# Kernel tuning notes

Measured on AMD Instinct MI355X. Metric: run time of the kernel, lower is better.

Reference implementation:

```python
import jax, jax.numpy as jnp
import numpy as np

CUTOFF = 10.0
EPS_W = 1e-5
EPS_LN = 1e-5

def _silu(v):
    return v * jax.nn.sigmoid(v)

def setup_inputs() -> dict:
    key = jax.random.key(0)
    ks = jax.random.split(key, 12)
    N, E, H, R = 50000, 300000, 256, 64
    s = lambda fan_in: 1.0 / np.sqrt(fan_in)
    inp = {
        'x': jax.random.normal(ks[0], (N, H), jnp.float32),
        'edge_index': jax.random.randint(ks[1], (2, E), 0, N, jnp.int64 if jax.config.jax_enable_x64 else jnp.int32),
        'distances': jax.random.uniform(ks[2], (E,), jnp.float32) * CUTOFF,
        'centers': jnp.linspace(0.0, CUTOFF, R).astype(jnp.float32),
        'widths': jnp.full((R,), CUTOFF / R, jnp.float32),
        'rbf_w1': jax.random.normal(ks[3], (R, R), jnp.float32) * s(R),
        'rbf_b1': jnp.zeros((R,), jnp.float32),
        'rbf_w2': jax.random.normal(ks[4], (R, R), jnp.float32) * s(R),
        'rbf_b2': jnp.zeros((R,), jnp.float32),
        'filt_w1': jax.random.normal(ks[5], (R, H), jnp.float32) * s(R),
        'filt_b1': jnp.zeros((H,), jnp.float32),
        'filt_w2': jax.random.normal(ks[6], (H, H), jnp.float32) * s(H),
        'filt_b2': jnp.zeros((H,), jnp.float32),
        'filt_w3': jax.random.normal(ks[7], (H, H), jnp.float32) * s(H),
        'filt_b3': jnp.zeros((H,), jnp.float32),
        'node_w': jax.random.normal(ks[8], (H, H), jnp.float32) * s(H),
        'node_b': jnp.zeros((H,), jnp.float32),
        'ln_g': jnp.ones((H,), jnp.float32),
        'ln_b': jnp.zeros((H,), jnp.float32),
        'gate_w': jax.random.normal(ks[9], (H, H), jnp.float32) * s(H),
        'gate_b': jnp.zeros((H,), jnp.float32),
    }
    return inp

def reference(x, edge_index, distances, centers, widths,
              rbf_w1, rbf_b1, rbf_w2, rbf_b2,
              filt_w1, filt_b1, filt_w2, filt_b2, filt_w3, filt_b3,
              node_w, node_b, ln_g, ln_b, gate_w, gate_b):
    # LearnableRBF: envelope * gaussian basis, then 2-layer SiLU proj
    d = distances
    env = 0.5 * (jnp.cos(d * jnp.pi / CUTOFF) + 1.0) * (d < CUTOFF).astype(x.dtype)  # [E]
    rbf = jnp.exp(-0.5 * ((d[:, None] - centers) / (jnp.abs(widths) + EPS_W)) ** 2)   # [E,R]
    r = rbf * env[:, None]
    r = _silu(r @ rbf_w1 + rbf_b1) @ rbf_w2 + rbf_b2                                  # [E,R]
    # filter network: Lin-SiLU-Lin-SiLU-Lin
    W = _silu(r @ filt_w1 + filt_b1)
    W = _silu(W @ filt_w2 + filt_b2) @ filt_w3 + filt_b3                              # [E,H]
    # gather -> modulate -> scatter-add (CFConv messaging)
    row, col = edge_index[0], edge_index[1]
    msg = (x[col] @ node_w + node_b) * W                                              # [E,H]
    agg = jax.ops.segment_sum(msg, row, num_segments=x.shape[0])                      # [N,H]
    h = x + agg
    mu = jnp.mean(h, axis=-1, keepdims=True)
    var = jnp.var(h, axis=-1, keepdims=True)
    out = (h - mu) / jnp.sqrt(var + EPS_LN) * ln_g + ln_b
    return out * jax.nn.sigmoid(out @ gate_w + gate_b)
```

## Files before the change

kernel.cpp:

```cpp
#include <hip/hip_runtime.h>
#include <hip/hip_bf16.h>
#include <math.h>

typedef __attribute__((ext_vector_type(8))) short bf16x8;
typedef __attribute__((ext_vector_type(4))) float f32x4;
typedef unsigned short ushort_t;

constexpr float F_CUTOFF = 10.0f;
constexpr float F_EPS_W  = 1e-5f;
constexpr float F_EPS_LN = 1e-5f;
constexpr float F_PI     = 3.14159265358979323846f;

__device__ __forceinline__ float silu_f(float v)   { return v / (1.0f + __expf(-v)); }
__device__ __forceinline__ float sigmoid_f(float v){ return 1.0f / (1.0f + __expf(-v)); }

__device__ __forceinline__ ushort_t f2bf(float f) {
    union { __hip_bfloat16 h; ushort_t u; } v; v.h = __float2bfloat16(f); return v.u;
}
__device__ __forceinline__ float bf2f(ushort_t u) {
    union { __hip_bfloat16 h; ushort_t u; } v; v.u = u; return __bfloat162float(v.h);
}

__device__ __forceinline__ float f4c(const float4& v, int q) {
    return q == 0 ? v.x : q == 1 ? v.y : q == 2 ? v.z : v.w;
}

__global__ void count_kernel(const int* __restrict__ eidx, int* __restrict__ cnt, int E)
{
    int e = blockIdx.x * 256 + threadIdx.x;
    if (e < E) atomicAdd(&cnt[eidx[e]], 1);
}

__global__ __launch_bounds__(1024)
void scan_kernel(const int* __restrict__ cnt, int* __restrict__ start,
                 int* __restrict__ cursor, int N)
{
    __shared__ int part[1024];
    const int tid = threadIdx.x;
    const int C = (N + 1023) >> 10;
    const int base = tid * C;
    int s = 0;
    for (int i = 0; i < C; ++i) {
        int idx = base + i;
        if (idx < N) s += cnt[idx];
    }
    part[tid] = s;
    __syncthreads();
    for (int off = 1; off < 1024; off <<= 1) {
        int v = (tid >= off) ? part[tid - off] : 0;
        __syncthreads();
        part[tid] += v;
        __syncthreads();
    }
    int run = part[tid] - s;
    for (int i = 0; i < C; ++i) {
        int idx = base + i;
        if (idx < N) {
            start[idx]  = run;
            cursor[idx] = run;
            run += cnt[idx];
        }
    }
    if (tid == 1023) start[N] = part[1023];
}

__global__ void scatter_kernel(const int* __restrict__ eidx, int* __restrict__ cursor,
                               int* __restrict__ slot, int E)
{
    int e = blockIdx.x * 256 + threadIdx.x;
    if (e < E) slot[e] = atomicAdd(&cursor[eidx[e]], 1);
}

__global__ void cvt_transpose_kernel(const float* __restrict__ in, ushort_t* __restrict__ out,
                                     int K, int N, int logK)
{
    int idx = blockIdx.x * 256 + threadIdx.x;
    if (idx >= K * N) return;
    int n = idx >> logK;
    int k = idx & (K - 1);
    out[idx] = f2bf(in[k * N + n]);
}

__global__ void combine_w_kernel(const float* __restrict__ w2, const float* __restrict__ fw1,
                                 ushort_t* __restrict__ out)
{
    int idx = blockIdx.x * 256 + threadIdx.x;
    int c = idx >> 6, j = idx & 63;
    float s = 0.f;
    #pragma unroll 8
    for (int n = 0; n < 64; ++n) s += w2[j * 64 + n] * fw1[n * 256 + c];
    out[idx] = f2bf(s);
}

__global__ void combine_b_kernel(const float* __restrict__ b2, const float* __restrict__ fw1,
                                 const float* __restrict__ fb1, float* __restrict__ out)
{
    int c = threadIdx.x;
    float s = fb1[c];
    #pragma unroll 8
    for (int n = 0; n < 64; ++n) s += b2[n] * fw1[n * 256 + c];
    out[c] = s;
}

__global__ __launch_bounds__(256)
void gemm256_bf16_kernel(const float* __restrict__ A, const float* __restrict__ Wm,
                         const float* __restrict__ bias, ushort_t* __restrict__ out, int M)
{
    __shared__ float4 As4[64][64];
    const int t = threadIdx.x;
    const int row0 = blockIdx.x * 64;

    #pragma unroll
    for (int i = 0; i < 16; ++i) {
        int flat = t + i * 256;
        int r = flat >> 6, k4 = flat & 63;
        int row = row0 + r;
        float4 v = make_float4(0.f, 0.f, 0.f, 0.f);
        if (row < M) v = reinterpret_cast<const float4*>(A)[row * 64 + k4];
        As4[r][k4] = v;
    }
    __syncthreads();

    const int jt  = t & 31;
    const int et  = t >> 5;
    const int j04 = jt * 2;
    const int r0  = et * 8;

    float acc[8][8];
    #pragma unroll
    for (int r = 0; r < 8; ++r)
        #pragma unroll
        for (int c = 0; c < 8; ++c) acc[r][c] = 0.f;

    for (int k4 = 0; k4 < 64; ++k4) {
        float4 a4[8];
        #pragma unroll
        for (int r = 0; r < 8; ++r) a4[r] = As4[r0 + r][k4];
        #pragma unroll
        for (int q = 0; q < 4; ++q) {
            const int k = k4 * 4 + q;
            float4 b0 = reinterpret_cast<const float4*>(Wm)[k * 64 + j04];
            float4 b1 = reinterpret_cast<const float4*>(Wm)[k * 64 + j04 + 1];
            float bb[8] = {b0.x, b0.y, b0.z, b0.w, b1.x, b1.y, b1.z, b1.w};
            #pragma unroll
            for (int r = 0; r < 8; ++r) {
                float av = f4c(a4[r], q);
                #pragma unroll
                for (int c = 0; c < 8; ++c) acc[r][c] = fmaf(av, bb[c], acc[r][c]);
            }
        }
    }

    float4 bv0 = reinterpret_cast<const float4*>(bias)[j04];
    float4 bv1 = reinterpret_cast<const float4*>(bias)[j04 + 1];
    float bb[8] = {bv0.x, bv0.y, bv0.z, bv0.w, bv1.x, bv1.y, bv1.z, bv1.w};

    #pragma unroll
    for (int r = 0; r < 8; ++r) {
        int row = row0 + r0 + r;
        if (row >= M) continue;
        ushort_t o8[8];
        #pragma unroll
        for (int c = 0; c < 8; ++c) o8[c] = f2bf(acc[r][c] + bb[c]);
        *reinterpret_cast<uint4*>(out + (size_t)row * 256 + jt * 8) = *reinterpret_cast<uint4*>(o8);
    }
}

__global__ __launch_bounds__(256)
void gate_gemm_kernel(const float* __restrict__ A, const float* __restrict__ Wm,
                      const float* __restrict__ bias, float* __restrict__ out, int M)
{
    __shared__ float4 As4[64][64];
    const int t = threadIdx.x;
    const int row0 = blockIdx.x * 64;

    #pragma unroll
    for (int i = 0; i < 16; ++i) {
        int flat = t + i * 256;
        int r = flat >> 6, k4 = flat & 63;
        int row = row0 + r;
        float4 v = make_float4(0.f, 0.f, 0.f, 0.f);
        if (row < M) v = reinterpret_cast<const float4*>(A)[row * 64 + k4];
        As4[r][k4] = v;
    }
    __syncthreads();

    const int jt  = t & 31;
    const int et  = t >> 5;
    const int j04 = jt * 2;
    const int r0  = et * 8;

    float acc[8][8];
    #pragma unroll
    for (int r = 0; r < 8; ++r)
        #pragma unroll
        for (int c = 0; c < 8; ++c) acc[r][c] = 0.f;

    for (int k4 = 0; k4 < 64; ++k4) {
        float4 a4[8];
        #pragma unroll
        for (int r = 0; r < 8; ++r) a4[r] = As4[r0 + r][k4];
        #pragma unroll
        for (int q = 0; q < 4; ++q) {
            const int k = k4 * 4 + q;
            float4 b0 = reinterpret_cast<const float4*>(Wm)[k * 64 + j04];
            float4 b1 = reinterpret_cast<const float4*>(Wm)[k * 64 + j04 + 1];
            float bb[8] = {b0.x, b0.y, b0.z, b0.w, b1.x, b1.y, b1.z, b1.w};
            #pragma unroll
            for (int r = 0; r < 8; ++r) {
                float av = f4c(a4[r], q);
                #pragma unroll
                for (int c = 0; c < 8; ++c) acc[r][c] = fmaf(av, bb[c], acc[r][c]);
            }
        }
    }

    float4 bv0 = reinterpret_cast<const float4*>(bias)[j04];
    float4 bv1 = reinterpret_cast<const float4*>(bias)[j04 + 1];
    float bb[8] = {bv0.x, bv0.y, bv0.z, bv0.w, bv1.x, bv1.y, bv1.z, bv1.w};

    #pragma unroll
    for (int r = 0; r < 8; ++r) {
        int row = row0 + r0 + r;
        if (row >= M) continue;
        float4 a0 = As4[r0 + r][j04];
        float4 a1 = As4[r0 + r][j04 + 1];
        float aa[8] = {a0.x, a0.y, a0.z, a0.w, a1.x, a1.y, a1.z, a1.w};
        float o[8];
        #pragma unroll
        for (int c = 0; c < 8; ++c) o[c] = aa[c] * sigmoid_f(acc[r][c] + bb[c]);
        reinterpret_cast<float4*>(out)[row * 64 + j04]     = make_float4(o[0], o[1], o[2], o[3]);
        reinterpret_cast<float4*>(out)[row * 64 + j04 + 1] = make_float4(o[4], o[5], o[6], o[7]);
    }
}

template<int KS, int NT, bool SILU>
__device__ __forceinline__ void mlp_stage(const unsigned char* in, unsigned char* out,
                                          const ushort_t* __restrict__ Wt,
                                          const float* __restrict__ bias,
                                          int wn, int g, int q)
{
    constexpr int K = KS * 32;
    f32x4 acc[2][NT];
    #pragma unroll
    for (int mt = 0; mt < 2; ++mt)
        #pragma unroll
        for (int nt = 0; nt < NT; ++nt) acc[mt][nt] = (f32x4){0.f, 0.f, 0.f, 0.f};

    #pragma unroll
    for (int kk = 0; kk < KS; ++kk) {
        bf16x8 b[NT];
        #pragma unroll
        for (int nt = 0; nt < NT; ++nt) {
            int n = (wn * NT + nt) * 16 + q;
            b[nt] = *reinterpret_cast<const bf16x8*>(Wt + n * K + kk * 32 + g * 8);
        }
        bf16x8 a[2];
        #pragma unroll
        for (int mt = 0; mt < 2; ++mt) {
            int m = mt * 16 + q;
            int unit = (4 * kk + g) ^ (m & 7);
            a[mt] = *reinterpret_cast<const bf16x8*>(in + m * 512 + unit * 16);
        }
        #pragma unroll
        for (int mt = 0; mt < 2; ++mt)
            #pragma unroll
            for (int nt = 0; nt < NT; ++nt)
                acc[mt][nt] = __builtin_amdgcn_mfma_f32_16x16x32_bf16(a[mt], b[nt], acc[mt][nt], 0, 0, 0);
    }

    const bool evenq = (q & 1) == 0;
    #pragma unroll
    for (int nt = 0; nt < NT; ++nt) {
        int n0  = (wn * NT + nt) * 16 + q;
        int n_e = n0 & ~1;
        float2 bv = *reinterpret_cast<const float2*>(bias + n_e);
        #pragma unroll
        for (int mt = 0; mt < 2; ++mt) {
            float v[4], p[4];
            #pragma unroll
            for (int r = 0; r < 4; ++r) { v[r] = acc[mt][nt][r]; p[r] = __shfl_xor(v[r], 1, 64); }
            #pragma unroll
            for (int rr = 0; rr < 2; ++rr) {
                int r = evenq ? rr : (2 + rr);
                float lo = (evenq ? v[r] : p[r]) + bv.x;
                float hi = (evenq ? p[r] : v[r]) + bv.y;
                if (SILU) { lo = silu_f(lo); hi = silu_f(hi); }
                int m = mt * 16 + 4 * g + r;
                unsigned u = (unsigned)f2bf(lo) | ((unsigned)f2bf(hi) << 16);
                int byte = m * 512 + (((n_e >> 3) ^ (m & 7)) << 4) + ((n_e & 7) * 2);
                *reinterpret_cast<unsigned*>(out + byte) = u;
            }
        }
    }
}

template<int TWO>
__global__ __launch_bounds__(256, 4)
void edge_mfma_kernel(const float* __restrict__ dist, const int* __restrict__ eidx,
                      const float* __restrict__ centers, const float* __restrict__ widths,
                      const ushort_t* __restrict__ wt_rbf1, const float* __restrict__ rbf_b1,
                      const ushort_t* __restrict__ wt_comb, const float* __restrict__ b_comb,
                      const ushort_t* __restrict__ wt_f2, const float* __restrict__ filt_b2,
                      const ushort_t* __restrict__ wt_f3, const float* __restrict__ filt_b3,
                      const ushort_t* __restrict__ y, const int* __restrict__ slot,
                      float* __restrict__ dst, int E)
{
    __shared__ __align__(16) unsigned char bufA[16384];
    __shared__ __align__(16) unsigned char bufB[16384];
    __shared__ int rs_s[32];

    const int t  = threadIdx.x;
    const int e0 = blockIdx.x * 32;
    const int wn   = t >> 6;
    const int lane = t & 63;
    const int g = lane >> 4, q = lane & 15;

    if (t < 32) {
        int ge = e0 + t;
        if (TWO) rs_s[t] = (ge < E) ? slot[ge] : 0;
        else     rs_s[t] = (ge < E) ? eidx[ge] : 0;
    }

    const int e_own  = t >> 3;
    const int chunk  = t & 7;
    const int ge_own = e0 + e_own;
    const int col_own = (ge_own < E) ? eidx[E + ge_own] : 0;
    uint4 yv[4];
    #pragma unroll
    for (int i = 0; i < 4; ++i)
        yv[i] = *reinterpret_cast<const uint4*>(y + (size_t)col_own * 256 + (i * 8 + chunk) * 8);

    {
        float d = (ge_own < E) ? dist[ge_own] : F_CUTOFF;
        float env = (d < F_CUTOFF) ? 0.5f * (__cosf(d * (F_PI / F_CUTOFF)) + 1.0f) : 0.0f;
        unsigned char* rowp = bufA + e_own * 512;
        int k0 = chunk * 8;
        #pragma unroll
        for (int i = 0; i < 4; ++i) {
            int n = k0 + 2 * i;
            float c0 = centers[n],     w0 = fabsf(widths[n]) + F_EPS_W;
            float c1 = centers[n + 1], w1 = fabsf(widths[n + 1]) + F_EPS_W;
            float z0 = (d - c0) / w0, z1 = (d - c1) / w1;
            float r0 = env * __expf(-0.5f * z0 * z0);
            float r1 = env * __expf(-0.5f * z1 * z1);
            unsigned u = (unsigned)f2bf(r0) | ((unsigned)f2bf(r1) << 16);
            int byte = (((n >> 3) ^ (e_own & 7)) << 4) + ((n & 7) * 2);
            *reinterpret_cast<unsigned*>(rowp + byte) = u;
        }
    }
    __syncthreads();

    mlp_stage<2, 1, true>(bufA, bufB, wt_rbf1, rbf_b1, wn, g, q);
    __syncthreads();
    mlp_stage<2, 4, true>(bufB, bufA, wt_comb, b_comb, wn, g, q);
    __syncthreads();
    mlp_stage<8, 4, true>(bufA, bufB, wt_f2, filt_b2, wn, g, q);
    __syncthreads();

    #pragma unroll
    for (int i = 0; i < 4; ++i)
        *reinterpret_cast<uint4*>(bufA + e_own * 512 + (i * 8 + chunk) * 16) = yv[i];
    __syncthreads();

    {
        f32x4 acc[2][4];
        #pragma unroll
        for (int mt = 0; mt < 2; ++mt)
            #pragma unroll
            for (int nt = 0; nt < 4; ++nt) acc[mt][nt] = (f32x4){0.f, 0.f, 0.f, 0.f};

        #pragma unroll
        for (int kk = 0; kk < 8; ++kk) {
            bf16x8 b[4];
            #pragma unroll
            for (int nt = 0; nt < 4; ++nt) {
                int n = (wn * 4 + nt) * 16 + q;
                b[nt] = *reinterpret_cast<const bf16x8*>(wt_f3 + n * 256 + kk * 32 + g * 8);
            }
            bf16x8 a[2];
            #pragma unroll
            for (int mt = 0; mt < 2; ++mt) {
                int m = mt * 16 + q;
                int unit = (4 * kk + g) ^ (m & 7);
                a[mt] = *reinterpret_cast<const bf16x8*>(bufB + m * 512 + unit * 16);
            }
            #pragma unroll
            for (int mt = 0; mt < 2; ++mt)
                #pragma unroll
                for (int nt = 0; nt < 4; ++nt)
                    acc[mt][nt] = __builtin_amdgcn_mfma_f32_16x16x32_bf16(a[mt], b[nt], acc[mt][nt], 0, 0, 0);
        }

        float bn[4];
        int   nn[4];
        #pragma unroll
        for (int nt = 0; nt < 4; ++nt) { nn[nt] = (wn * 4 + nt) * 16 + q; bn[nt] = filt_b3[nn[nt]]; }

        #pragma unroll
        for (int mt = 0; mt < 2; ++mt) {
            #pragma unroll
            for (int r = 0; r < 4; ++r) {
                int m  = mt * 16 + 4 * g + r;
                int ge = e0 + m;
                if (ge < E) {
                    const unsigned char* yrow = bufA + m * 512;
                    if (TWO) {
                        float* mrow = dst + (size_t)rs_s[m] * 256;
                        #pragma unroll
                        for (int nt = 0; nt < 4; ++nt) {
                            float wv = acc[mt][nt][r] + bn[nt];
                            float yvv = bf2f(*reinterpret_cast<const ushort_t*>(yrow + nn[nt] * 2));
                            mrow[nn[nt]] = wv * yvv;
                        }
                    } else {
                        float* arow = dst + (size_t)rs_s[m] * 256;
                        #pragma unroll
                        for (int nt = 0; nt < 4; ++nt) {
                            float wv = acc[mt][nt][r] + bn[nt];
                            float yvv = bf2f(*reinterpret_cast<const ushort_t*>(yrow + nn[nt] * 2));
                            unsafeAtomicAdd(&arow[nn[nt]], wv * yvv);
                        }
                    }
                }
            }
        }
    }
}

__global__ __launch_bounds__(256)
void agg_ln_kernel(const float* __restrict__ x, const float* __restrict__ msg,
                   const int* __restrict__ start,
                   const float* __restrict__ g, const float* __restrict__ b,
                   float* __restrict__ out0, int N)
{
    int lane = threadIdx.x & 63;
    int row  = blockIdx.x * 4 + (threadIdx.x >> 6);
    if (row >= N) return;
    int s0 = start[row], s1 = start[row + 1];
    float4 h = reinterpret_cast<const float4*>(x)[row * 64 + lane];
    for (int s = s0; s < s1; ++s) {
        float4 m = reinterpret_cast<const float4*>(msg)[(size_t)s * 64 + lane];
        h.x += m.x; h.y += m.y; h.z += m.z; h.w += m.w;
    }
    float su  = h.x + h.y + h.z + h.w;
    float s2 = h.x * h.x + h.y * h.y + h.z * h.z + h.w * h.w;
    #pragma unroll
    for (int off = 32; off > 0; off >>= 1) {
        su += __shfl_xor(su, off, 64);
        s2 += __shfl_xor(s2, off, 64);
    }
    float mu  = su * (1.0f / 256.0f);
    float var = s2 * (1.0f / 256.0f) - mu * mu;
    float inv = rsqrtf(var + F_EPS_LN);
    float4 gv = reinterpret_cast<const float4*>(g)[lane];
    float4 bv = reinterpret_cast<const float4*>(b)[lane];
    float4 o;
    o.x = (h.x - mu) * inv * gv.x + bv.x;
    o.y = (h.y - mu) * inv * gv.y + bv.y;
    o.z = (h.z - mu) * inv * gv.z + bv.z;
    o.w = (h.w - mu) * inv * gv.w + bv.w;
    reinterpret_cast<float4*>(out0)[row * 64 + lane] = o;
}

__global__ __launch_bounds__(256)
void ln_kernel(const float* __restrict__ x, const float* __restrict__ agg,
               const float* __restrict__ g, const float* __restrict__ b,
               float* __restrict__ out0, int N)
{
    int lane = threadIdx.x & 63;
    int row  = blockIdx.x * 4 + (threadIdx.x >> 6);
    if (row >= N) return;
    float4 hx = reinterpret_cast<const float4*>(x)[row * 64 + lane];
    float4 ha = reinterpret_cast<const float4*>(agg)[row * 64 + lane];
    float4 h  = make_float4(hx.x + ha.x, hx.y + ha.y, hx.z + ha.z, hx.w + ha.w);
    float s  = h.x + h.y + h.z + h.w;
    float s2 = h.x * h.x + h.y * h.y + h.z * h.z + h.w * h.w;
    #pragma unroll
    for (int off = 32; off > 0; off >>= 1) {
        s  += __shfl_xor(s,  off, 64);
        s2 += __shfl_xor(s2, off, 64);
    }
    float mu  = s * (1.0f / 256.0f);
    float var = s2 * (1.0f / 256.0f) - mu * mu;
    float inv = rsqrtf(var + F_EPS_LN);
    float4 gv = reinterpret_cast<const float4*>(g)[lane];
    float4 bv = reinterpret_cast<const float4*>(b)[lane];
    float4 o;
    o.x = (h.x - mu) * inv * gv.x + bv.x;
    o.y = (h.y - mu) * inv * gv.y + bv.y;
    o.z = (h.z - mu) * inv * gv.z + bv.z;
    o.w = (h.w - mu) * inv * gv.w + bv.w;
    reinterpret_cast<float4*>(out0)[row * 64 + lane] = o;
}

extern "C" void kernel_launch(void* const* d_in, const int* in_sizes, int n_in,
                              void* d_out, int out_size, void* d_ws, size_t ws_size,
                              hipStream_t stream)
{
    const float* x       = (const float*)d_in[0];
    const int*   eidx    = (const int*)  d_in[1];
    const float* dist    = (const float*)d_in[2];
    const float* centers = (const float*)d_in[3];
    const float* widths  = (const float*)d_in[4];
    const float* rbf_w1  = (const float*)d_in[5];
    const float* rbf_b1  = (const float*)d_in[6];
    const float* rbf_w2  = (const float*)d_in[7];
    const float* rbf_b2  = (const float*)d_in[8];
    const float* filt_w1 = (const float*)d_in[9];
    const float* filt_b1 = (const float*)d_in[10];
    const float* filt_w2 = (const float*)d_in[11];
    const float* filt_b2 = (const float*)d_in[12];
    const float* filt_w3 = (const float*)d_in[13];
    const float* filt_b3 = (const float*)d_in[14];
    const float* node_w  = (const float*)d_in[15];
    const float* node_b  = (const float*)d_in[16];
    const float* ln_g    = (const float*)d_in[17];
    const float* ln_b    = (const float*)d_in[18];
    const float* gate_w  = (const float*)d_in[19];
    const float* gate_b  = (const float*)d_in[20];

    const int N = in_sizes[0] / 256;
    const int E = in_sizes[2];

    char* wsb = (char*)d_ws;
    size_t off = 0;
    auto alloc = [&](size_t bytes, size_t align) -> char* {
        off = (off + align - 1) & ~(align - 1);
        char* p = wsb + off;
        off += bytes;
        return p;
    };
    ushort_t* y_bf  = (ushort_t*)alloc((size_t)N * 256 * 2, 16);
    ushort_t* wt1   = (ushort_t*)alloc(64 * 64 * 2, 16);
    ushort_t* wcomb = (ushort_t*)alloc(256 * 64 * 2, 16);
    ushort_t* wf2   = (ushort_t*)alloc(256 * 256 * 2, 16);
    ushort_t* wf3   = (ushort_t*)alloc(256 * 256 * 2, 16);
    float*    bcomb = (float*)   alloc(256 * 4, 16);
    int*      cnt   = (int*)     alloc((size_t)N * 4, 16);
    int*      start = (int*)     alloc(((size_t)N + 1) * 4, 16);
    int*      cursor= (int*)     alloc((size_t)N * 4, 16);
    int*      slot  = (int*)     alloc((size_t)E * 4, 16);
    float*    msg   = (float*)   alloc((size_t)E * 256 * 4, 1024);
    const bool two_phase = (off <= ws_size);

    dim3 b256(256);

    cvt_transpose_kernel<<<dim3((64 * 64 + 255) / 256),   b256, 0, stream>>>(rbf_w1,  wt1, 64, 64, 6);
    combine_w_kernel<<<dim3(64), b256, 0, stream>>>(rbf_w2, filt_w1, wcomb);
    combine_b_kernel<<<dim3(1), b256, 0, stream>>>(rbf_b2, filt_w1, filt_b1, bcomb);
    cvt_transpose_kernel<<<dim3((256 * 256 + 255) / 256), b256, 0, stream>>>(filt_w2, wf2, 256, 256, 8);
    cvt_transpose_kernel<<<dim3((256 * 256 + 255) / 256), b256, 0, stream>>>(filt_w3, wf3, 256, 256, 8);

    gemm256_bf16_kernel<<<dim3((N + 63) / 64), b256, 0, stream>>>(x, node_w, node_b, y_bf, N);

    if (two_phase) {
        hipMemsetAsync(cnt, 0, (size_t)N * 4, stream);
        count_kernel<<<dim3((E + 255) / 256), b256, 0, stream>>>(eidx, cnt, E);
        scan_kernel<<<dim3(1), 1024, 0, stream>>>(cnt, start, cursor, N);
        scatter_kernel<<<dim3((E + 255) / 256), b256, 0, stream>>>(eidx, cursor, slot, E);

        edge_mfma_kernel<1><<<dim3((E + 31) / 32), b256, 0, stream>>>(
            dist, eidx, centers, widths,
            wt1, rbf_b1, wcomb, bcomb,
            wf2, filt_b2, wf3, filt_b3,
            y_bf, slot, msg, E);

        agg_ln_kernel<<<dim3((N + 3) / 4), b256, 0, stream>>>(x, msg, start, ln_g, ln_b, (float*)d_out, N);
    } else {
        hipMemsetAsync(d_out, 0, (size_t)out_size * sizeof(float), stream);
        edge_mfma_kernel<0><<<dim3((E + 31) / 32), b256, 0, stream>>>(
            dist, eidx, centers, widths,
            wt1, rbf_b1, wcomb, bcomb,
            wf2, filt_b2, wf3, filt_b3,
            y_bf, slot, (float*)d_out, E);
        ln_kernel<<<dim3((N + 3) / 4), b256, 0, stream>>>(x, (float*)d_out, ln_g, ln_b, (float*)d_out, N);
    }

    gate_gemm_kernel<<<dim3((N + 63) / 64), b256, 0, stream>>>((float*)d_out, gate_w, gate_b, (float*)d_out, N);
}
```

Baseline: 822.8 us.

## Split fused edge MLP into staged GEMM kernels with bf16 intermediates

Splits the monolithic per-edge kernel into an RBF/first-layer kernel that writes bf16 features, then two standalone 64-row tiled MFMA GEMM kernels with double-buffered LDS for the 256x256 filter layers. The last GEMM writes the bf16 filter into CSR-sorted slots, and the aggregation kernel gathers y by a sorted column array to do the multiply there. This replaces the fp32 message buffer with bf16 and gives larger GEMM tiles with better weight reuse. In exchange it adds extra global round trips of E x 256 bf16 intermediates and more kernel launches.

```diff
diff --git a/kernel.cpp b/kernel.cpp
--- a/kernel.cpp
+++ b/kernel.cpp
@@ -18,7 +18,7 @@
     union { __hip_bfloat16 h; ushort_t u; } v; v.h = __float2bfloat16(f); return v.u;
 }
 __device__ __forceinline__ float bf2f(ushort_t u) {
-    union { __hip_bfloat16 h; ushort_t u; } v; v.u = u; return __bfloat162float(v.h);
+    union { unsigned u; float f; } v; v.u = ((unsigned)u) << 16; return v.f;
 }
 
 __device__ __forceinline__ float f4c(const float4& v, int q) {
@@ -32,8 +32,8 @@
 }
 
 __global__ __launch_bounds__(1024)
-void scan_kernel(const int* __restrict__ cnt, int* __restrict__ start,
-                 int* __restrict__ cursor, int N)
+void scan_kernel(int* __restrict__ cnt ,
+                 int* __restrict__ start, int N)
 {
     __shared__ int part[1024];
     const int tid = threadIdx.x;
@@ -56,19 +56,24 @@
     for (int i = 0; i < C; ++i) {
         int idx = base + i;
         if (idx < N) {
-            start[idx]  = run;
-            cursor[idx] = run;
-            run += cnt[idx];
+            int c = cnt[idx];
+            start[idx] = run;
+            cnt[idx]   = run;
+            run += c;
         }
     }
     if (tid == 1023) start[N] = part[1023];
 }
 
 __global__ void scatter_kernel(const int* __restrict__ eidx, int* __restrict__ cursor,
-                               int* __restrict__ slot, int E)
+                               int* __restrict__ slot, int* __restrict__ colos, int E)
 {
     int e = blockIdx.x * 256 + threadIdx.x;
-    if (e < E) slot[e] = atomicAdd(&cursor[eidx[e]], 1);
+    if (e < E) {
+        int s = atomicAdd(&cursor[eidx[e]], 1);
+        slot[e] = s;
+        colos[s] = eidx[E + e];
+    }
 }
 
 __global__ void cvt_transpose_kernel(const float* __restrict__ in, ushort_t* __restrict__ out,
@@ -295,20 +300,15 @@
     }
 }
 
-template<int TWO>
 __global__ __launch_bounds__(256, 4)
-void edge_mfma_kernel(const float* __restrict__ dist, const int* __restrict__ eidx,
-                      const float* __restrict__ centers, const float* __restrict__ widths,
-                      const ushort_t* __restrict__ wt_rbf1, const float* __restrict__ rbf_b1,
-                      const ushort_t* __restrict__ wt_comb, const float* __restrict__ b_comb,
-                      const ushort_t* __restrict__ wt_f2, const float* __restrict__ filt_b2,
-                      const ushort_t* __restrict__ wt_f3, const float* __restrict__ filt_b3,
-                      const ushort_t* __restrict__ y, const int* __restrict__ slot,
-                      float* __restrict__ dst, int E)
+void rbf_f1_kernel(const float* __restrict__ dist,
+                   const float* __restrict__ centers, const float* __restrict__ widths,
+                   const ushort_t* __restrict__ wt_rbf1, const float* __restrict__ rbf_b1,
+                   const ushort_t* __restrict__ wt_comb, const float* __restrict__ b_comb,
+                   ushort_t* __restrict__ f1, int E)
 {
     __shared__ __align__(16) unsigned char bufA[16384];
     __shared__ __align__(16) unsigned char bufB[16384];
-    __shared__ int rs_s[32];
 
     const int t  = threadIdx.x;
     const int e0 = blockIdx.x * 32;
@@ -316,20 +316,9 @@
     const int lane = t & 63;
     const int g = lane >> 4, q = lane & 15;
 
-    if (t < 32) {
-        int ge = e0 + t;
-        if (TWO) rs_s[t] = (ge < E) ? slot[ge] : 0;
-        else     rs_s[t] = (ge < E) ? eidx[ge] : 0;
-    }
-
     const int e_own  = t >> 3;
     const int chunk  = t & 7;
     const int ge_own = e0 + e_own;
-    const int col_own = (ge_own < E) ? eidx[E + ge_own] : 0;
-    uint4 yv[4];
-    #pragma unroll
-    for (int i = 0; i < 4; ++i)
-        yv[i] = *reinterpret_cast<const uint4*>(y + (size_t)col_own * 256 + (i * 8 + chunk) * 8);
 
     {
         float d = (ge_own < E) ? dist[ge_own] : F_CUTOFF;
@@ -355,73 +344,115 @@
     __syncthreads();
     mlp_stage<2, 4, true>(bufB, bufA, wt_comb, b_comb, wn, g, q);
     __syncthreads();
-    mlp_stage<8, 4, true>(bufA, bufB, wt_f2, filt_b2, wn, g, q);
-    __syncthreads();
-
-    #pragma unroll
-    for (int i = 0; i < 4; ++i)
-        *reinterpret_cast<uint4*>(bufA + e_own * 512 + (i * 8 + chunk) * 16) = yv[i];
-    __syncthreads();
-
-    {
-        f32x4 acc[2][4];
-        #pragma unroll
-        for (int mt = 0; mt < 2; ++mt)
-            #pragma unroll
-            for (int nt = 0; nt < 4; ++nt) acc[mt][nt] = (f32x4){0.f, 0.f, 0.f, 0.f};
-
-        #pragma unroll
-        for (int kk = 0; kk < 8; ++kk) {
+
+    if (ge_own < E) {
+        #pragma unroll
+        for (int i = 0; i < 4; ++i) {
+            int c = chunk + i * 8;
+            int u = (c ^ (e_own & 7)) | (c & 24);
+            u = (c & 24) | ((c ^ (e_own & 7)) & 7);
+            uint4 v = *reinterpret_cast<const uint4*>(bufA + e_own * 512 + u * 16);
+            *reinterpret_cast<uint4*>(f1 + (size_t)ge_own * 256 + c * 8) = v;
+        }
+    }
+}
+
+template<int EPI>
+__global__ __launch_bounds__(256, 3)
+void gemm_stage_kernel(const ushort_t* __restrict__ A, const ushort_t* __restrict__ Wt,
+                       const float* __restrict__ bias, ushort_t* __restrict__ out,
+                       const int* __restrict__ slot, int M)
+{
+    __shared__ __align__(16) unsigned char sbuf[2][8192];
+    __shared__ int slot_s[64];
+
+    const int t  = threadIdx.x;
+    const int m0 = blockIdx.x * 64;
+    const int wn   = t >> 6;
+    const int lane = t & 63;
+    const int g = lane >> 4, q = lane & 15;
+
+    if (EPI == 1 && t < 64) {
+        int gm = m0 + t;
+        slot_s[t] = (gm < M) ? slot[gm] : 0;
+    }
+
+    const int s0r = t >> 3,        s0u = t & 7;
+    const int s1r = (t + 256) >> 3, s1u = t & 7;
+    const ushort_t* src0base = A + (size_t)((m0 + s0r < M) ? (m0 + s0r) : (M - 1)) * 256 + ((s0u ^ (s0r & 7)) * 8);
+    const ushort_t* src1base = A + (size_t)((m0 + s1r < M) ? (m0 + s1r) : (M - 1)) * 256 + ((s1u ^ (s1r & 7)) * 8);
+
+    uint4 p0 = *reinterpret_cast<const uint4*>(src0base);
+    uint4 p1 = *reinterpret_cast<const uint4*>(src1base);
+    *reinterpret_cast<uint4*>(&sbuf[0][t * 16])         = p0;
+    *reinterpret_cast<uint4*>(&sbuf[0][(t + 256) * 16]) = p1;
+    __syncthreads();
+
+    f32x4 acc[4][4];
+    #pragma unroll
+    for (int mt = 0; mt < 4; ++mt)
+        #pragma unroll
+        for (int nt = 0; nt < 4; ++nt) acc[mt][nt] = (f32x4){0.f, 0.f, 0.f, 0.f};
+
+    for (int kt = 0; kt < 4; ++kt) {
+        const int cur = kt & 1;
+        uint4 nx0, nx1;
+        if (kt < 3) {
+            nx0 = *reinterpret_cast<const uint4*>(src0base + (kt + 1) * 64);
+            nx1 = *reinterpret_cast<const uint4*>(src1base + (kt + 1) * 64);
+        }
+        #pragma unroll
+        for (int ks = 0; ks < 2; ++ks) {
             bf16x8 b[4];
             #pragma unroll
             for (int nt = 0; nt < 4; ++nt) {
-                int n = (wn * 4 + nt) * 16 + q;
-                b[nt] = *reinterpret_cast<const bf16x8*>(wt_f3 + n * 256 + kk * 32 + g * 8);
-            }
-            bf16x8 a[2];
-            #pragma unroll
-            for (int mt = 0; mt < 2; ++mt) {
-                int m = mt * 16 + q;
-                int unit = (4 * kk + g) ^ (m & 7);
-                a[mt] = *reinterpret_cast<const bf16x8*>(bufB + m * 512 + unit * 16);
-            }
-            #pragma unroll
-            for (int mt = 0; mt < 2; ++mt)
+                int n = wn * 64 + nt * 16 + q;
+                b[nt] = *reinterpret_cast<const bf16x8*>(Wt + (size_t)n * 256 + kt * 64 + ks * 32 + g * 8);
+            }
+            bf16x8 a[4];
+            #pragma unroll
+            for (int mt = 0; mt < 4; ++mt) {
+                int r = mt * 16 + q;
+                int u = (ks * 4 + g) ^ (r & 7);
+                a[mt] = *reinterpret_cast<const bf16x8*>(&sbuf[cur][r * 128 + u * 16]);
+            }
+            #pragma unroll
+            for (int mt = 0; mt < 4; ++mt)
                 #pragma unroll
                 for (int nt = 0; nt < 4; ++nt)
                     acc[mt][nt] = __builtin_amdgcn_mfma_f32_16x16x32_bf16(a[mt], b[nt], acc[mt][nt], 0, 0, 0);
         }
-
-        float bn[4];
-        int   nn[4];
-        #pragma unroll
-        for (int nt = 0; nt < 4; ++nt) { nn[nt] = (wn * 4 + nt) * 16 + q; bn[nt] = filt_b3[nn[nt]]; }
-
-        #pragma unroll
-        for (int mt = 0; mt < 2; ++mt) {
-            #pragma unroll
-            for (int r = 0; r < 4; ++r) {
-                int m  = mt * 16 + 4 * g + r;
-                int ge = e0 + m;
-                if (ge < E) {
-                    const unsigned char* yrow = bufA + m * 512;
-                    if (TWO) {
-                        float* mrow = dst + (size_t)rs_s[m] * 256;
-                        #pragma unroll
-                        for (int nt = 0; nt < 4; ++nt) {
-                            float wv = acc[mt][nt][r] + bn[nt];
-                            float yvv = bf2f(*reinterpret_cast<const ushort_t*>(yrow + nn[nt] * 2));
-                            mrow[nn[nt]] = wv * yvv;
-                        }
-                    } else {
-                        float* arow = dst + (size_t)rs_s[m] * 256;
-                        #pragma unroll
-                        for (int nt = 0; nt < 4; ++nt) {
-                            float wv = acc[mt][nt][r] + bn[nt];
-                            float yvv = bf2f(*reinterpret_cast<const ushort_t*>(yrow + nn[nt] * 2));
-                            unsafeAtomicAdd(&arow[nn[nt]], wv * yvv);
-                        }
-                    }
+        __syncthreads();
+        if (kt < 3) {
+            *reinterpret_cast<uint4*>(&sbuf[cur ^ 1][t * 16])         = nx0;
+            *reinterpret_cast<uint4*>(&sbuf[cur ^ 1][(t + 256) * 16]) = nx1;
+            __syncthreads();
+        }
+    }
+
+    const bool evenq = (q & 1) == 0;
+    #pragma unroll
+    for (int nt = 0; nt < 4; ++nt) {
+        int n0  = wn * 64 + nt * 16 + q;
+        int n_e = n0 & ~1;
+        float2 bv = *reinterpret_cast<const float2*>(bias + n_e);
+        #pragma unroll
+        for (int mt = 0; mt < 4; ++mt) {
+            float v[4], p[4];
+            #pragma unroll
+            for (int r = 0; r < 4; ++r) { v[r] = acc[mt][nt][r]; p[r] = __shfl_xor(v[r], 1, 64); }
+            #pragma unroll
+            for (int rr = 0; rr < 2; ++rr) {
+                int r = evenq ? rr : (2 + rr);
+                float lo = (evenq ? v[r] : p[r]) + bv.x;
+                float hi = (evenq ? p[r] : v[r]) + bv.y;
+                if (EPI == 0) { lo = silu_f(lo); hi = silu_f(hi); }
+                int mloc = mt * 16 + 4 * g + r;
+                int grow = m0 + mloc;
+                if (grow < M) {
+                    int drow = (EPI == 1) ? slot_s[mloc] : grow;
+                    unsigned u = (unsigned)f2bf(lo) | ((unsigned)f2bf(hi) << 16);
+                    *reinterpret_cast<unsigned*>(out + (size_t)drow * 256 + n_e) = u;
                 }
             }
         }
@@ -429,22 +460,29 @@
 }
 
 __global__ __launch_bounds__(256)
-void agg_ln_kernel(const float* __restrict__ x, const float* __restrict__ msg,
-                   const int* __restrict__ start,
-                   const float* __restrict__ g, const float* __restrict__ b,
-                   float* __restrict__ out0, int N)
+void agg_ln2_kernel(const float* __restrict__ x, const ushort_t* __restrict__ Wf,
+                    const int* __restrict__ start, const int* __restrict__ colos,
+                    const ushort_t* __restrict__ y,
+                    const float* __restrict__ g, const float* __restrict__ b,
+                    float* __restrict__ out0, int N)
 {
     int lane = threadIdx.x & 63;
     int row  = blockIdx.x * 4 + (threadIdx.x >> 6);
     if (row >= N) return;
     int s0 = start[row], s1 = start[row + 1];
-    float4 h = reinterpret_cast<const float4*>(x)[row * 64 + lane];
+    float4 hx = reinterpret_cast<const float4*>(x)[row * 64 + lane];
+    float hh[4] = {hx.x, hx.y, hx.z, hx.w};
     for (int s = s0; s < s1; ++s) {
-        float4 m = reinterpret_cast<const float4*>(msg)[(size_t)s * 64 + lane];
-        h.x += m.x; h.y += m.y; h.z += m.z; h.w += m.w;
-    }
-    float su  = h.x + h.y + h.z + h.w;
-    float s2 = h.x * h.x + h.y * h.y + h.z * h.z + h.w * h.w;
+        uint2 wv = *reinterpret_cast<const uint2*>(Wf + (size_t)s * 256 + lane * 4);
+        int c = colos[s];
+        uint2 yv = *reinterpret_cast<const uint2*>(y + (size_t)c * 256 + lane * 4);
+        hh[0] += bf2f((ushort_t)(wv.x & 0xffff)) * bf2f((ushort_t)(yv.x & 0xffff));
+        hh[1] += bf2f((ushort_t)(wv.x >> 16))    * bf2f((ushort_t)(yv.x >> 16));
+        hh[2] += bf2f((ushort_t)(wv.y & 0xffff)) * bf2f((ushort_t)(yv.y & 0xffff));
+        hh[3] += bf2f((ushort_t)(wv.y >> 16))    * bf2f((ushort_t)(yv.y >> 16));
+    }
+    float su = hh[0] + hh[1] + hh[2] + hh[3];
+    float s2 = hh[0]*hh[0] + hh[1]*hh[1] + hh[2]*hh[2] + hh[3]*hh[3];
     #pragma unroll
     for (int off = 32; off > 0; off >>= 1) {
         su += __shfl_xor(su, off, 64);
@@ -456,11 +494,131 @@
     float4 gv = reinterpret_cast<const float4*>(g)[lane];
     float4 bv = reinterpret_cast<const float4*>(b)[lane];
     float4 o;
-    o.x = (h.x - mu) * inv * gv.x + bv.x;
-    o.y = (h.y - mu) * inv * gv.y + bv.y;
-    o.z = (h.z - mu) * inv * gv.z + bv.z;
-    o.w = (h.w - mu) * inv * gv.w + bv.w;
+    o.x = (hh[0] - mu) * inv * gv.x + bv.x;
+    o.y = (hh[1] - mu) * inv * gv.y + bv.y;
+    o.z = (hh[2] - mu) * inv * gv.z + bv.z;
+    o.w = (hh[3] - mu) * inv * gv.w + bv.w;
     reinterpret_cast<float4*>(out0)[row * 64 + lane] = o;
+}
+
+__global__ __launch_bounds__(256, 4)
+void edge_atomic_kernel(const float* __restrict__ dist, const int* __restrict__ eidx,
+                        const float* __restrict__ centers, const float* __restrict__ widths,
+                        const ushort_t* __restrict__ wt_rbf1, const float* __restrict__ rbf_b1,
+                        const ushort_t* __restrict__ wt_comb, const float* __restrict__ b_comb,
+                        const ushort_t* __restrict__ wt_f2, const float* __restrict__ filt_b2,
+                        const ushort_t* __restrict__ wt_f3, const float* __restrict__ filt_b3,
+                        const ushort_t* __restrict__ y, float* __restrict__ agg, int E)
+{
+    __shared__ __align__(16) unsigned char bufA[16384];
+    __shared__ __align__(16) unsigned char bufB[16384];
+    __shared__ int rs_s[32];
+
+    const int t  = threadIdx.x;
+    const int e0 = blockIdx.x * 32;
+    const int wn   = t >> 6;
+    const int lane = t & 63;
+    const int g = lane >> 4, q = lane & 15;
+
+    if (t < 32) {
+        int ge = e0 + t;
+        rs_s[t] = (ge < E) ? eidx[ge] : 0;
+    }
+
+    const int e_own  = t >> 3;
+    const int chunk  = t & 7;
+    const int ge_own = e0 + e_own;
+    const int col_own = (ge_own < E) ? eidx[E + ge_own] : 0;
+    uint4 yv[4];
+    #pragma unroll
+    for (int i = 0; i < 4; ++i)
+        yv[i] = *reinterpret_cast<const uint4*>(y + (size_t)col_own * 256 + (i * 8 + chunk) * 8);
+
+    {
+        float d = (ge_own < E) ? dist[ge_own] : F_CUTOFF;
+        float env = (d < F_CUTOFF) ? 0.5f * (__cosf(d * (F_PI / F_CUTOFF)) + 1.0f) : 0.0f;
+        unsigned char* rowp = bufA + e_own * 512;
+        int k0 = chunk * 8;
+        #pragma unroll
+        for (int i = 0; i < 4; ++i) {
+            int n = k0 + 2 * i;
+            float c0 = centers[n],     w0 = fabsf(widths[n]) + F_EPS_W;
+            float c1 = centers[n + 1], w1 = fabsf(widths[n + 1]) + F_EPS_W;
+            float z0 = (d - c0) / w0, z1 = (d - c1) / w1;
+            float r0 = env * __expf(-0.5f * z0 * z0);
+            float r1 = env * __expf(-0.5f * z1 * z1);
+            unsigned u = (unsigned)f2bf(r0) | ((unsigned)f2bf(r1) << 16);
+            int byte = (((n >> 3) ^ (e_own & 7)) << 4) + ((n & 7) * 2);
+            *reinterpret_cast<unsigned*>(rowp + byte) = u;
+        }
+    }
+    __syncthreads();
+
+    mlp_stage<2, 1, true>(bufA, bufB, wt_rbf1, rbf_b1, wn, g, q);
+    __syncthreads();
+    mlp_stage<2, 4, true>(bufB, bufA, wt_comb, b_comb, wn, g, q);
+    __syncthreads();
+    mlp_stage<8, 4, true>(bufA, bufB, wt_f2, filt_b2, wn, g, q);
+    __syncthreads();
+
+    #pragma unroll
+    for (int i = 0; i < 4; ++i)
+        *reinterpret_cast<uint4*>(bufA + e_own * 512 + (i * 8 + chunk) * 16) = yv[i];
+    __syncthreads();
+
+    {
+        f32x4 acc[2][4];
+        #pragma unroll
+        for (int mt = 0; mt < 2; ++mt)
+            #pragma unroll
+            for (int nt = 0; nt < 4; ++nt) acc[mt][nt] = (f32x4){0.f, 0.f, 0.f, 0.f};
+
+        #pragma unroll
+        for (int kk = 0; kk < 8; ++kk) {
+            bf16x8 b[4];
+            #pragma unroll
+            for (int nt = 0; nt < 4; ++nt) {
+                int n = (wn * 4 + nt) * 16 + q;
+                b[nt] = *reinterpret_cast<const bf16x8*>(wt_f3 + n * 256 + kk * 32 + g * 8);
+            }
+            bf16x8 a[2];
+            #pragma unroll
+            for (int mt = 0; mt < 2; ++mt) {
+                int m = mt * 16 + q;
+                int unit = (4 * kk + g) ^ (m & 7);
+                a[mt] = *reinterpret_cast<const bf16x8*>(bufB + m * 512 + unit * 16);
+            }
+            #pragma unroll
+            for (int mt = 0; mt < 2; ++mt)
+                #pragma unroll
+                for (int nt = 0; nt < 4; ++nt)
+                    acc[mt][nt] = __builtin_amdgcn_mfma_f32_16x16x32_bf16(a[mt], b[nt], acc[mt][nt], 0, 0, 0);
+        }
+
+        float bn[4];
+        int   nn[4];
+        #pragma unroll
+        for (int nt = 0; nt < 4; ++nt) { nn[nt] = (wn * 4 + nt) * 16 + q; bn[nt] = filt_b3[nn[nt]]; }
+
+        #pragma unroll
+        for (int mt = 0; mt < 2; ++mt) {
+            #pragma unroll
+            for (int r = 0; r < 4; ++r) {
+                int m  = mt * 16 + 4 * g + r;
+                int ge = e0 + m;
+                if (ge < E) {
+                    const unsigned char* yrow = bufA + m * 512;
+                    float* arow = agg + (size_t)rs_s[m] * 256;
+                    #pragma unroll
+                    for (int nt = 0; nt < 4; ++nt) {
+                        float wv = acc[mt][nt][r] + bn[nt];
+                        float yvv = bf2f(*reinterpret_cast<const ushort_t*>(yrow + nn[nt] * 2));
+                        unsafeAtomicAdd(&arow[nn[nt]], wv * yvv);
+                    }
+                }
+            }
+        }
+    }
 }
 
 __global__ __launch_bounds__(256)
@@ -534,14 +692,16 @@
     ushort_t* y_bf  = (ushort_t*)alloc((size_t)N * 256 * 2, 16);
     ushort_t* wt1   = (ushort_t*)alloc(64 * 64 * 2, 16);
     ushort_t* wcomb = (ushort_t*)alloc(256 * 64 * 2, 16);
-    ushort_t* wf2   = (ushort_t*)alloc(256 * 256 * 2, 16);
-    ushort_t* wf3   = (ushort_t*)alloc(256 * 256 * 2, 16);
+    ushort_t* wf2t  = (ushort_t*)alloc(256 * 256 * 2, 16);
+    ushort_t* wf3t  = (ushort_t*)alloc(256 * 256 * 2, 16);
     float*    bcomb = (float*)   alloc(256 * 4, 16);
     int*      cnt   = (int*)     alloc((size_t)N * 4, 16);
     int*      start = (int*)     alloc(((size_t)N + 1) * 4, 16);
-    int*      cursor= (int*)     alloc((size_t)N * 4, 16);
     int*      slot  = (int*)     alloc((size_t)E * 4, 16);
-    float*    msg   = (float*)   alloc((size_t)E * 256 * 4, 1024);
+    int*      colos = (int*)     alloc((size_t)E * 4, 16);
+    ushort_t* f1    = (ushort_t*)alloc((size_t)E * 256 * 2, 1024);
+    ushort_t* f2    = (ushort_t*)alloc((size_t)E * 256 * 2, 1024);
+    ushort_t* Wf    = f1;
     const bool two_phase = (off <= ws_size);
 
     dim3 b256(256);
@@ -549,31 +709,35 @@
     cvt_transpose_kernel<<<dim3((64 * 64 + 255) / 256),   b256, 0, stream>>>(rbf_w1,  wt1, 64, 64, 6);
     combine_w_kernel<<<dim3(64), b256, 0, stream>>>(rbf_w2, filt_w1, wcomb);
     combine_b_kernel<<<dim3(1), b256, 0, stream>>>(rbf_b2, filt_w1, filt_b1, bcomb);
-    cvt_transpose_kernel<<<dim3((256 * 256 + 255) / 256), b256, 0, stream>>>(filt_w2, wf2, 256, 256, 8);
-    cvt_transpose_kernel<<<dim3((256 * 256 + 255) / 256), b256, 0, stream>>>(filt_w3, wf3, 256, 256, 8);
+    cvt_transpose_kernel<<<dim3((256 * 256 + 255) / 256), b256, 0, stream>>>(filt_w2, wf2t, 256, 256, 8);
+    cvt_transpose_kernel<<<dim3((256 * 256 + 255) / 256), b256, 0, stream>>>(filt_w3, wf3t, 256, 256, 8);
 
     gemm256_bf16_kernel<<<dim3((N + 63) / 64), b256, 0, stream>>>(x, node_w, node_b, y_bf, N);
 
     if (two_phase) {
         hipMemsetAsync(cnt, 0, (size_t)N * 4, stream);
         count_kernel<<<dim3((E + 255) / 256), b256, 0, stream>>>(eidx, cnt, E);
-        scan_kernel<<<dim3(1), 1024, 0, stream>>>(cnt, start, cursor, N);
-        scatter_kernel<<<dim3((E + 255) / 256), b256, 0, stream>>>(eidx, cursor, slot, E);
-
-        edge_mfma_kernel<1><<<dim3((E + 31) / 32), b256, 0, stream>>>(
+        scan_kernel<<<dim3(1), 1024, 0, stream>>>(cnt, start, N);
+        scatter_kernel<<<dim3((E + 255) / 256), b256, 0, stream>>>(eidx, cnt, slot, colos, E);
+
+        rbf_f1_kernel<<<dim3((E + 31) / 32), b256, 0, stream>>>(
+            dist, centers, widths, wt1, rbf_b1, wcomb, bcomb, f1, E);
+
+        gemm_stage_kernel<0><<<dim3((E + 63) / 64), b256, 0, stream>>>(
+            f1, wf2t, filt_b2, f2, nullptr, E);
+
+        gemm_stage_kernel<1><<<dim3((E + 63) / 64), b256, 0, stream>>>(
+            f2, wf3t, filt_b3, Wf, slot, E);
+
+        agg_ln2_kernel<<<dim3((N + 3) / 4), b256, 0, stream>>>(
+            x, Wf, start, colos, y_bf, ln_g, ln_b, (float*)d_out, N);
+    } else {
+        hipMemsetAsync(d_out, 0, (size_t)out_size * sizeof(float), stream);
+        edge_atomic_kernel<<<dim3((E + 31) / 32), b256, 0, stream>>>(
             dist, eidx, centers, widths,
             wt1, rbf_b1, wcomb, bcomb,
-            wf2, filt_b2, wf3, filt_b3,
-            y_bf, slot, msg, E);
-
-        agg_ln_kernel<<<dim3((N + 3) / 4), b256, 0, stream>>>(x, msg, start, ln_g, ln_b, (float*)d_out, N);
-    } else {
-        hipMemsetAsync(d_out, 0, (size_t)out_size * sizeof(float), stream);
-        edge_mfma_kernel<0><<<dim3((E + 31) / 32), b256, 0, stream>>>(
-            dist, eidx, centers, widths,
-            wt1, rbf_b1, wcomb, bcomb,
-            wf2, filt_b2, wf3, filt_b3,
-            y_bf, slot, (float*)d_out, E);
+            wf2t, filt_b2, wf3t, filt_b3,
+            y_bf, (float*)d_out, E);
         ln_kernel<<<dim3((N + 3) / 4), b256, 0, stream>>>(x, (float*)d_out, ln_g, ln_b, (float*)d_out, N);
     }
 
```

Result: no change. 822.8 us (-0.0%).
